# Performance work log

Measured on AMD Instinct MI355X. Metric: run time of the kernel, lower is better.

## Reference

```python
import jax, jax.numpy as jnp
import numpy as np

N = 50000
E = 800000
IN_DIM, HID, HEADS, OUT = 128, 32, 8, 64
NEG_SLOPE = 0.2
EPS = 1e-16


def setup_inputs() -> dict:
    key = jax.random.key(0)
    ks = jax.random.split(key, 10)
    return {
        "x": jax.random.normal(ks[0], (N, IN_DIM), dtype=jnp.float32),
        "edge_index": jax.random.randint(ks[1], (2, E), 0, N, dtype=jnp.int64)
        if jax.config.jax_enable_x64 else jax.random.randint(ks[1], (2, E), 0, N, dtype=jnp.int32),
        "W1": jax.random.normal(ks[2], (HEADS * HID, IN_DIM), dtype=jnp.float32) * 0.1,
        "att_src1": jax.random.normal(ks[3], (HEADS, HID), dtype=jnp.float32) * 0.1,
        "att_dst1": jax.random.normal(ks[4], (HEADS, HID), dtype=jnp.float32) * 0.1,
        "b1": jnp.zeros((HEADS * HID,), dtype=jnp.float32),
        "W2": jax.random.normal(ks[5], (OUT, HEADS * HID), dtype=jnp.float32) * 0.1,
        "att_src2": jax.random.normal(ks[6], (1, OUT), dtype=jnp.float32) * 0.1,
        "att_dst2": jax.random.normal(ks[7], (1, OUT), dtype=jnp.float32) * 0.1,
        "b2": jnp.zeros((OUT,), dtype=jnp.float32),
    }


def _gat_conv(x, src, dst, W, att_src, att_dst, bias, heads, out_dim, concat, n_nodes):
    # x: [N, F_in]; W: [heads*out_dim, F_in]; att_*: [heads, out_dim]
    h = (x @ W.T).reshape(n_nodes, heads, out_dim)      # [N, H, D]
    a_src = jnp.einsum('nhd,hd->nh', h, att_src)         # [N, H]
    a_dst = jnp.einsum('nhd,hd->nh', h, att_dst)
    alpha = jax.nn.leaky_relu(a_src[src] + a_dst[dst], NEG_SLOPE)  # [E, H]
    # segment softmax over edges grouped by destination node
    m = jax.ops.segment_max(alpha, dst, num_segments=n_nodes)
    alpha = jnp.exp(alpha - m[dst])
    s = jax.ops.segment_sum(alpha, dst, num_segments=n_nodes)
    alpha = alpha / (s[dst] + EPS)
    msg = h[src] * alpha[:, :, None]                     # [E, H, D]
    out = jax.ops.segment_sum(msg, dst, num_segments=n_nodes)  # [N, H, D]
    if concat:
        out = out.reshape(n_nodes, heads * out_dim)
    else:
        out = out.mean(axis=1)
    return out + bias


def reference(x, edge_index, W1, att_src1, att_dst1, b1, W2, att_src2, att_dst2, b2):
    n = x.shape[0]
    loop = jnp.arange(n, dtype=edge_index.dtype)
    src = jnp.concatenate([edge_index[0], loop])  # PyG add_self_loops=True
    dst = jnp.concatenate([edge_index[1], loop])
    h = _gat_conv(x, src, dst, W1, att_src1, att_dst1, b1, HEADS, HID, True, n)
    h = jax.nn.relu(h)
    out = _gat_conv(h, src, dst, W2, att_src2, att_dst2, b2, 1, OUT, False, n)
    return out
```

## Files before the change

kernel.cpp:

```cpp
#include <hip/hip_runtime.h>
#include <hip/hip_fp16.h>

#define NN 50000
#define EE 800000
#define ET (EE + NN)
#define IND 128
#define F1 256
#define H1 8
#define D1 32
#define F2 64
#define NEG 0.2f
#define EPSV 1e-16f

#define MG2 391
#define SCB ((ET + 2047) / 2048)
#define BCAP 64

typedef _Float16 half8_t __attribute__((ext_vector_type(8)));
typedef _Float16 half4_t __attribute__((ext_vector_type(4)));
typedef float floatx4 __attribute__((ext_vector_type(4)));

#define W1N4 (256 * 128 / 4)
#define W2N4 (64 * 256 / 4)
#define DEG4 (NN / 4)
#define CVTN (W1N4 + W2N4 + DEG4 + 256)
__global__ void k_cvtW(const float* __restrict__ w1, const float* __restrict__ w2,
                       __half* __restrict__ w1p, __half* __restrict__ w2h,
                       int* __restrict__ deg, const float* __restrict__ as2w,
                       const float* __restrict__ ad2w, float* __restrict__ v2s,
                       float* __restrict__ v2d) {
  int i = blockIdx.x * blockDim.x + threadIdx.x;
  if (i < W1N4) {
    float4 v = *(const float4*)(w1 + (size_t)i * 4);
    int col = i >> 5;
    int kb = (i * 4) & 127;
    int by = col >> 7, t = (col >> 4) & 7, ar = col & 15;
    int kk = kb >> 5, ag = (kb >> 3) & 3, j = kb & 7;
    int fid = (by * 8 + t) * 4 + kk;
    int lane = ag * 16 + ar;
    __half2 p0 = __floats2half2_rn(v.x, v.y);
    __half2 p1 = __floats2half2_rn(v.z, v.w);
    float2 st;
    *(__half2*)&st.x = p0;
    *(__half2*)&st.y = p1;
    *(float2*)(w1p + fid * 512 + lane * 8 + j) = st;
    return;
  }
  i -= W1N4;
  if (i < W2N4) {
    float4 v = *(const float4*)(w2 + (size_t)i * 4);
    __half2 p0 = __floats2half2_rn(v.x, v.y);
    __half2 p1 = __floats2half2_rn(v.z, v.w);
    float2 st;
    *(__half2*)&st.x = p0;
    *(__half2*)&st.y = p1;
    *(float2*)(w2h + (size_t)i * 4) = st;
    return;
  }
  i -= W2N4;
  if (i < DEG4) {
    int4 z = make_int4(0, 0, 0, 0);
    *(int4*)(deg + i * 4) = z;
    return;
  }
  i -= DEG4;
  if (i < 256) {
    float s = 0.f, d = 0.f;
#pragma unroll 8
    for (int c = 0; c < 64; ++c) {
      float w = w2[c * 256 + i];
      s = fmaf(w, as2w[c], s);
      d = fmaf(w, ad2w[c], d);
    }
    v2s[i] = s;
    v2d[i] = d;
  }
}

__global__ __launch_bounds__(256) void k_scg1(const int* __restrict__ ei,
    int* __restrict__ deg, unsigned short* __restrict__ bkt,
    const float* __restrict__ A, const __half* __restrict__ Bp,
    __half* __restrict__ Ch, const float* __restrict__ as1w,
    const float* __restrict__ ad1w, float* __restrict__ as1,
    float* __restrict__ ad1) {
  if (blockIdx.x >= 2 * MG2) {
    int base = (blockIdx.x - 2 * MG2) * 2048 + threadIdx.x * 8;
    if (base >= ET) return;
    if (base + 8 <= EE) {
      int4 s0 = *(const int4*)(ei + base);
      int4 s1 = *(const int4*)(ei + base + 4);
      int4 d0 = *(const int4*)(ei + EE + base);
      int4 d1 = *(const int4*)(ei + EE + base + 4);
      int s[8] = {s0.x, s0.y, s0.z, s0.w, s1.x, s1.y, s1.z, s1.w};
      int d[8] = {d0.x, d0.y, d0.z, d0.w, d1.x, d1.y, d1.z, d1.w};
#pragma unroll
      for (int j = 0; j < 8; ++j) {
        int pos = atomicAdd(&deg[d[j]], 1);
        if (pos < BCAP) bkt[(d[j] << 6) + pos] = (unsigned short)s[j];
      }
    } else {
      for (int j = 0; j < 8; ++j) {
        int e = base + j;
        if (e >= ET) break;
        int ss, dd;
        if (e < EE) { ss = ei[e]; dd = ei[EE + e]; }
        else        { ss = e - EE; dd = ss; }
        int pos = atomicAdd(&deg[dd], 1);
        if (pos < BCAP) bkt[(dd << 6) + pos] = (unsigned short)ss;
      }
    }
    return;
  }
  int bx = blockIdx.x % MG2, by = blockIdx.x / MG2;
  int tid = threadIdx.x;
  int wv = tid >> 6, lane = tid & 63;
  int m0 = bx * 128 + wv * 16;
  int ar = lane & 15, ag = lane >> 4;
  int r0 = m0 + ar;       if (r0 >= NN) r0 = NN - 1;
  int r1 = m0 + 64 + ar;  if (r1 >= NN) r1 = NN - 1;
  const float* A0 = A + (size_t)r0 * IND + ag * 8;
  const float* A1 = A + (size_t)r1 * IND + ag * 8;
  floatx4 acc[2][8];
#pragma unroll
  for (int rt = 0; rt < 2; ++rt)
#pragma unroll
    for (int t = 0; t < 8; ++t) acc[rt][t] = (floatx4){0.f, 0.f, 0.f, 0.f};
#pragma unroll
  for (int kk = 0; kk < 4; ++kk) {
    int k0 = kk * 32;
    float4 a00 = *(const float4*)(A0 + k0);
    float4 a01 = *(const float4*)(A0 + k0 + 4);
    float4 a10 = *(const float4*)(A1 + k0);
    float4 a11 = *(const float4*)(A1 + k0 + 4);
    half8_t af0, af1;
    af0[0] = (_Float16)a00.x; af0[1] = (_Float16)a00.y;
    af0[2] = (_Float16)a00.z; af0[3] = (_Float16)a00.w;
    af0[4] = (_Float16)a01.x; af0[5] = (_Float16)a01.y;
    af0[6] = (_Float16)a01.z; af0[7] = (_Float16)a01.w;
    af1[0] = (_Float16)a10.x; af1[1] = (_Float16)a10.y;
    af1[2] = (_Float16)a10.z; af1[3] = (_Float16)a10.w;
    af1[4] = (_Float16)a11.x; af1[5] = (_Float16)a11.y;
    af1[6] = (_Float16)a11.z; af1[7] = (_Float16)a11.w;
#pragma unroll
    for (int t = 0; t < 8; ++t) {
      int fid = (by * 8 + t) * 4 + kk;
      half8_t bf = *(const half8_t*)(Bp + fid * 512 + lane * 8);
      acc[0][t] = __builtin_amdgcn_mfma_f32_16x16x32_f16(af0, bf, acc[0][t], 0, 0, 0);
      acc[1][t] = __builtin_amdgcn_mfma_f32_16x16x32_f16(af1, bf, acc[1][t], 0, 0, 0);
    }
  }
#pragma unroll
  for (int rt = 0; rt < 2; ++rt)
#pragma unroll
    for (int t = 0; t < 8; ++t) {
      int col = by * 128 + t * 16 + ar;
#pragma unroll
      for (int r = 0; r < 4; ++r) {
        int m = m0 + rt * 64 + ag * 4 + r;
        if (m < NN) Ch[(size_t)m * F1 + col] = __float2half(acc[rt][t][r]);
      }
    }
#pragma unroll
  for (int hp = 0; hp < 4; ++hp) {
    int head = by * 4 + hp;
    float sp[2][4] = {}, dp[2][4] = {};
#pragma unroll
    for (int th = 0; th < 2; ++th) {
      int t = 2 * hp + th;
      float ws = as1w[head * D1 + th * 16 + ar];
      float wd = ad1w[head * D1 + th * 16 + ar];
#pragma unroll
      for (int rt = 0; rt < 2; ++rt)
#pragma unroll
        for (int r = 0; r < 4; ++r) {
          sp[rt][r] = fmaf(acc[rt][t][r], ws, sp[rt][r]);
          dp[rt][r] = fmaf(acc[rt][t][r], wd, dp[rt][r]);
        }
    }
#pragma unroll
    for (int msk = 1; msk < 16; msk <<= 1)
#pragma unroll
      for (int rt = 0; rt < 2; ++rt)
#pragma unroll
        for (int r = 0; r < 4; ++r) {
          sp[rt][r] += __shfl_xor(sp[rt][r], msk);
          dp[rt][r] += __shfl_xor(dp[rt][r], msk);
        }
    if (ar == 0) {
#pragma unroll
      for (int rt = 0; rt < 2; ++rt)
#pragma unroll
        for (int r = 0; r < 4; ++r) {
          int m = m0 + rt * 64 + ag * 4 + r;
          if (m < NN) {
            as1[m * 8 + head] = sp[rt][r];
            ad1[m * 8 + head] = dp[rt][r];
          }
        }
    }
  }
}

__global__ __launch_bounds__(256) void k_agg1(const int* __restrict__ deg,
    const unsigned short* __restrict__ bkt, const __half* __restrict__ feat,
    const float* __restrict__ as_, const float* __restrict__ ad_,
    const float* __restrict__ bias, const float* __restrict__ v2s,
    const float* __restrict__ v2d, __half* __restrict__ outh,
    float* __restrict__ as2, float* __restrict__ ad2) {
  int wid = threadIdx.x >> 6;
  int lane = threadIdx.x & 63;
  int d = blockIdx.x * 4 + wid;
  if (d >= NN) return;
  const int b = lane >> 5;
  const int q = lane & 31;
  const int h = q >> 2;
  const int sw = lane >> 3;
  const int hw = lane & 7;
  const char* fb = (const char*)feat;
  float adw = ad_[d * 8 + hw];
  float acc[8] = {};
  float wsacc = 0.f;
  int p0 = d << 6;
  int dg = deg[d];
  int p1 = p0 + dg;
  int nfull = dg >> 3;
  int p = p0;
  for (int it = 0; it < nfull; ++it, p += 8) {
    int sW = bkt[p + sw];
    float t = as_[sW * 8 + hw] + adw;
    t = (t > 0.f) ? t : NEG * t;
    float w = __expf(t);
    wsacc += w;
    int wbits = __float_as_int(w);
#pragma unroll
    for (int i = 0; i < 4; ++i) {
      int slot = 2 * i + b;
      int se = __builtin_amdgcn_ds_bpermute(slot * 32, sW);
      float wv = __int_as_float(
          __builtin_amdgcn_ds_bpermute((slot * 8 + h) * 4, wbits));
      half8_t f = *(const half8_t*)(fb + ((se << 9) | (q << 4)));
#pragma unroll
      for (int j = 0; j < 8; ++j) acc[j] = fmaf(wv, (float)f[j], acc[j]);
    }
  }
  if (p < p1) {
    int pw = p + sw;
    bool v = pw < p1;
    int sW = bkt[v ? pw : (p1 - 1)];
    float t = as_[sW * 8 + hw] + adw;
    t = (t > 0.f) ? t : NEG * t;
    float w = v ? __expf(t) : 0.f;
    wsacc += w;
    int wbits = __float_as_int(w);
#pragma unroll
    for (int i = 0; i < 4; ++i) {
      int slot = 2 * i + b;
      int se = __builtin_amdgcn_ds_bpermute(slot * 32, sW);
      float wv = __int_as_float(
          __builtin_amdgcn_ds_bpermute((slot * 8 + h) * 4, wbits));
      half8_t f = *(const half8_t*)(fb + ((se << 9) | (q << 4)));
#pragma unroll
      for (int j = 0; j < 8; ++j) acc[j] = fmaf(wv, (float)f[j], acc[j]);
    }
  }
  wsacc += __shfl_xor(wsacc, 8);
  wsacc += __shfl_xor(wsacc, 16);
  wsacc += __shfl_xor(wsacc, 32);
  float wst = __int_as_float(
      __builtin_amdgcn_ds_bpermute(h * 4, __float_as_int(wsacc)));
#pragma unroll
  for (int j = 0; j < 8; ++j) acc[j] += __shfl_xor(acc[j], 32);
  float inv = 1.f / (wst + EPSV);
  float o[8];
#pragma unroll
  for (int j = 0; j < 8; ++j)
    o[j] = fmaxf(fmaf(acc[j], inv, 0.f) + bias[q * 8 + j], 0.f);
  if (b == 0) {
    __half2 packs[4];
#pragma unroll
    for (int j = 0; j < 8; j += 2)
      packs[j >> 1] = __floats2half2_rn(o[j], o[j + 1]);
    *(float4*)(outh + (size_t)d * 256 + q * 8) = *(float4*)packs;
  }
  float s2 = 0.f, d2 = 0.f;
#pragma unroll
  for (int j = 0; j < 8; ++j) {
    s2 = fmaf(o[j], v2s[q * 8 + j], s2);
    d2 = fmaf(o[j], v2d[q * 8 + j], d2);
  }
#pragma unroll
  for (int m = 1; m < 64; m <<= 1) {
    s2 += __shfl_xor(s2, m);
    d2 += __shfl_xor(d2, m);
  }
  if (lane == 0) { as2[d] = 0.5f * s2; ad2[d] = 0.5f * d2; }
}

__global__ __launch_bounds__(256) void k_g2(const __half* __restrict__ A,
    const __half* __restrict__ Bh, __half* __restrict__ Ch) {
  __shared__ __half Bs[64][256 + 8];
  int tid = threadIdx.x;
  const float4* src = (const float4*)Bh;
  for (int i = tid; i < 64 * 256 / 8; i += 256) {
    int row = i / 32, kc = i % 32;
    *(float4*)&Bs[row][kc * 8] = src[i];
  }
  __syncthreads();
  int wv = tid >> 6, lane = tid & 63;
  int m0 = blockIdx.x * 128 + wv * 16;
  int ar = lane & 15, ag = lane >> 4;
  int r0 = m0 + ar;       if (r0 >= NN) r0 = NN - 1;
  int r1 = m0 + 64 + ar;  if (r1 >= NN) r1 = NN - 1;
  const __half* A0 = A + (size_t)r0 * F1 + ag * 8;
  const __half* A1 = A + (size_t)r1 * F1 + ag * 8;
  floatx4 acc[2][4];
#pragma unroll
  for (int rt = 0; rt < 2; ++rt)
#pragma unroll
    for (int t = 0; t < 4; ++t) acc[rt][t] = (floatx4){0.f, 0.f, 0.f, 0.f};
#pragma unroll
  for (int k0 = 0; k0 < F1; k0 += 32) {
    half8_t af0 = *(const half8_t*)(A0 + k0);
    half8_t af1 = *(const half8_t*)(A1 + k0);
#pragma unroll
    for (int t = 0; t < 4; ++t) {
      half8_t bf = *(const half8_t*)&Bs[t * 16 + ar][k0 + ag * 8];
      acc[0][t] = __builtin_amdgcn_mfma_f32_16x16x32_f16(af0, bf, acc[0][t], 0, 0, 0);
      acc[1][t] = __builtin_amdgcn_mfma_f32_16x16x32_f16(af1, bf, acc[1][t], 0, 0, 0);
    }
  }
#pragma unroll
  for (int rt = 0; rt < 2; ++rt)
#pragma unroll
    for (int t = 0; t < 4; ++t) {
      int col = t * 16 + ar;
#pragma unroll
      for (int r = 0; r < 4; ++r) {
        int m = m0 + rt * 64 + ag * 4 + r;
        if (m < NN) Ch[(size_t)m * F2 + col] = __float2half(acc[rt][t][r]);
      }
    }
}

__global__ __launch_bounds__(256) void k_agg2(const int* __restrict__ deg,
    const unsigned short* __restrict__ bkt, const __half* __restrict__ feat,
    const float* __restrict__ as_, const float* __restrict__ ad_,
    const float* __restrict__ bias, float* __restrict__ out) {
  int slice = blockIdx.x & 1;
  int chunk = blockIdx.x >> 1;
  int wid = threadIdx.x >> 6;
  int lane = threadIdx.x & 63;
  int d = chunk * 4 + wid;
  if (d >= NN) return;
  const int b = lane >> 3;
  const int q = lane & 7;
  const char* fb = (const char*)feat + (slice << 6);
  float adv = ad_[d];
  float a0 = 0.f, a1 = 0.f, a2 = 0.f, a3 = 0.f;
  float ws = 0.f;
  int p0 = d << 6;
  int dg = deg[d];
  int p1 = p0 + dg;
  int nfull = dg >> 3;
  int p = p0;
  for (int it = 0; it < nfull; ++it, p += 8) {
    int se = bkt[p + b];
    float t = as_[se] + adv;
    t = (t > 0.f) ? t : NEG * t;
    float w = __expf(t);
    ws += w;
    half4_t f = *(const half4_t*)(fb + ((se << 7) | (q << 3)));
    a0 = fmaf(w, (float)f[0], a0);
    a1 = fmaf(w, (float)f[1], a1);
    a2 = fmaf(w, (float)f[2], a2);
    a3 = fmaf(w, (float)f[3], a3);
  }
  if (p < p1) {
    int pe = p + b;
    bool v = pe < p1;
    int se = bkt[v ? pe : (p1 - 1)];
    float t = as_[se] + adv;
    t = (t > 0.f) ? t : NEG * t;
    float w = v ? __expf(t) : 0.f;
    ws += w;
    half4_t f = *(const half4_t*)(fb + ((se << 7) | (q << 3)));
    a0 = fmaf(w, (float)f[0], a0);
    a1 = fmaf(w, (float)f[1], a1);
    a2 = fmaf(w, (float)f[2], a2);
    a3 = fmaf(w, (float)f[3], a3);
  }
  ws += __shfl_xor(ws, 8); ws += __shfl_xor(ws, 16); ws += __shfl_xor(ws, 32);
  a0 += __shfl_xor(a0, 8); a0 += __shfl_xor(a0, 16); a0 += __shfl_xor(a0, 32);
  a1 += __shfl_xor(a1, 8); a1 += __shfl_xor(a1, 16); a1 += __shfl_xor(a1, 32);
  a2 += __shfl_xor(a2, 8); a2 += __shfl_xor(a2, 16); a2 += __shfl_xor(a2, 32);
  a3 += __shfl_xor(a3, 8); a3 += __shfl_xor(a3, 16); a3 += __shfl_xor(a3, 32);
  if (b == 0) {
    float inv = 1.f / (ws + EPSV);
    int d0 = slice * 32 + q * 4;
    float4 o;
    o.x = fmaf(a0, inv, bias[d0 + 0]);
    o.y = fmaf(a1, inv, bias[d0 + 1]);
    o.z = fmaf(a2, inv, bias[d0 + 2]);
    o.w = fmaf(a3, inv, bias[d0 + 3]);
    *(float4*)(out + (size_t)d * 64 + d0) = o;
  }
}

extern "C" void kernel_launch(void* const* d_in, const int* in_sizes, int n_in,
                              void* d_out, int out_size, void* d_ws, size_t ws_size,
                              hipStream_t stream) {
  const float* x    = (const float*)d_in[0];
  const int*   ei   = (const int*)d_in[1];
  const float* W1   = (const float*)d_in[2];
  const float* as1w = (const float*)d_in[3];
  const float* ad1w = (const float*)d_in[4];
  const float* b1   = (const float*)d_in[5];
  const float* W2   = (const float*)d_in[6];
  const float* as2w = (const float*)d_in[7];
  const float* ad2w = (const float*)d_in[8];
  const float* b2   = (const float*)d_in[9];
  float* out = (float*)d_out;

  char* W = (char*)d_ws;
  __half* h1h = (__half*)W; W += (size_t)NN * 256 * 2;
  __half* h2h = (__half*)W; W += (size_t)NN * 256 * 2;
  __half* hmh = (__half*)W; W += (size_t)NN * 64 * 2;
  __half* W1p = (__half*)W; W += 256 * 128 * 2;
  __half* W2h = (__half*)W; W += 64 * 256 * 2;
  float* as1 = (float*)W; W += (size_t)NN * 8 * 4;
  float* ad1 = (float*)W; W += (size_t)NN * 8 * 4;
  float* as2 = (float*)W; W += (size_t)NN * 4;
  float* ad2 = (float*)W; W += (size_t)NN * 4;
  float* v2s = (float*)W; W += 256 * 4;
  float* v2d = (float*)W; W += 256 * 4;
  int* deg    = (int*)W;  W += (size_t)NN * 4;
  unsigned short* bkt = (unsigned short*)W; W += (size_t)NN * BCAP * 2;

  k_cvtW<<<(CVTN + 255) / 256, 256, 0, stream>>>(W1, W2, W1p, W2h, deg,
                                                 as2w, ad2w, v2s, v2d);
  k_scg1<<<2 * MG2 + SCB, 256, 0, stream>>>(ei, deg, bkt, x, W1p, h1h,
                                            as1w, ad1w, as1, ad1);
  k_agg1<<<(NN + 3) / 4, 256, 0, stream>>>(deg, bkt, h1h, as1, ad1, b1,
                                           v2s, v2d, h2h, as2, ad2);
  k_g2<<<MG2, 256, 0, stream>>>(h2h, W2h, hmh);
  k_agg2<<<2 * ((NN + 3) / 4), 256, 0, stream>>>(deg, bkt, hmh, as2, ad2, b2, out);
}
```

Before: 195.4 us.

## Pre-bin edges by destination range before bucket scatter; widen agg2 to full rows

Adds a k_bin pass that groups edges into 8 destination-range bins using block-local counts and global cursors, packing dst and src into one 32-bit word. The bucket-scatter blocks in k_scg1 then walk each bin, so the degree atomics and bucket writes for neighbouring blocks hit a narrower address range. The aim is better L2 locality for those atomics, paid for by an extra kernel launch and a round trip through the bin buffer. Separately, k_agg2 now has each wave handle all 64 output features with 8-wide half loads instead of splitting every node across two blocks, which halves the index and attention loads per node but doubles the register accumulators.

```diff
diff --git a/kernel.cpp b/kernel.cpp
--- a/kernel.cpp
+++ b/kernel.cpp
@@ -13,22 +13,26 @@
 #define EPSV 1e-16f
 
 #define MG2 391
-#define SCB ((ET + 2047) / 2048)
 #define BCAP 64
+#define NBIN 8
+#define DPB 6250
+#define BINCAP 114688
+#define SB2 56
+#define NSC (NBIN * SB2)
+#define BINB ((ET + 1023) / 1024)
 
 typedef _Float16 half8_t __attribute__((ext_vector_type(8)));
-typedef _Float16 half4_t __attribute__((ext_vector_type(4)));
 typedef float floatx4 __attribute__((ext_vector_type(4)));
 
 #define W1N4 (256 * 128 / 4)
 #define W2N4 (64 * 256 / 4)
 #define DEG4 (NN / 4)
-#define CVTN (W1N4 + W2N4 + DEG4 + 256)
+#define CVTN (W1N4 + W2N4 + DEG4 + 256 + 8)
 __global__ void k_cvtW(const float* __restrict__ w1, const float* __restrict__ w2,
                        __half* __restrict__ w1p, __half* __restrict__ w2h,
                        int* __restrict__ deg, const float* __restrict__ as2w,
                        const float* __restrict__ ad2w, float* __restrict__ v2s,
-                       float* __restrict__ v2d) {
+                       float* __restrict__ v2d, int* __restrict__ gcur) {
   int i = blockIdx.x * blockDim.x + threadIdx.x;
   if (i < W1N4) {
     float4 v = *(const float4*)(w1 + (size_t)i * 4);
@@ -74,44 +78,89 @@
     }
     v2s[i] = s;
     v2d[i] = d;
-  }
-}
-
-__global__ __launch_bounds__(256) void k_scg1(const int* __restrict__ ei,
-    int* __restrict__ deg, unsigned short* __restrict__ bkt,
-    const float* __restrict__ A, const __half* __restrict__ Bp,
-    __half* __restrict__ Ch, const float* __restrict__ as1w,
-    const float* __restrict__ ad1w, float* __restrict__ as1,
-    float* __restrict__ ad1) {
-  if (blockIdx.x >= 2 * MG2) {
-    int base = (blockIdx.x - 2 * MG2) * 2048 + threadIdx.x * 8;
-    if (base >= ET) return;
-    if (base + 8 <= EE) {
-      int4 s0 = *(const int4*)(ei + base);
-      int4 s1 = *(const int4*)(ei + base + 4);
-      int4 d0 = *(const int4*)(ei + EE + base);
-      int4 d1 = *(const int4*)(ei + EE + base + 4);
-      int s[8] = {s0.x, s0.y, s0.z, s0.w, s1.x, s1.y, s1.z, s1.w};
-      int d[8] = {d0.x, d0.y, d0.z, d0.w, d1.x, d1.y, d1.z, d1.w};
+    return;
+  }
+  i -= 256;
+  if (i < 8) gcur[i] = 0;
+}
+
+__global__ __launch_bounds__(256) void k_bin(const int* __restrict__ ei,
+    int* __restrict__ gcur, unsigned int* __restrict__ binbuf) {
+  __shared__ int lcnt[NBIN], lbase[NBIN];
+  if (threadIdx.x < NBIN) lcnt[threadIdx.x] = 0;
+  __syncthreads();
+  int base = blockIdx.x * 1024 + threadIdx.x * 4;
+  int s[4], d[4], bin[4], lpos[4];
+  int nv = 0;
+  if (base + 4 <= EE) {
+    int4 sv = *(const int4*)(ei + base);
+    int4 dv = *(const int4*)(ei + EE + base);
+    s[0] = sv.x; s[1] = sv.y; s[2] = sv.z; s[3] = sv.w;
+    d[0] = dv.x; d[1] = dv.y; d[2] = dv.z; d[3] = dv.w;
+    nv = 4;
+  } else {
+    for (int j = 0; j < 4; ++j) {
+      int e = base + j;
+      if (e < ET) {
+        if (e < EE) { s[nv] = ei[e]; d[nv] = ei[EE + e]; }
+        else        { s[nv] = e - EE; d[nv] = s[nv]; }
+        ++nv;
+      }
+    }
+  }
+  for (int j = 0; j < nv; ++j) {
+    bin[j] = d[j] / DPB;
+    lpos[j] = atomicAdd(&lcnt[bin[j]], 1);
+  }
+  __syncthreads();
+  if (threadIdx.x < NBIN)
+    lbase[threadIdx.x] = atomicAdd(&gcur[threadIdx.x], lcnt[threadIdx.x]);
+  __syncthreads();
+  for (int j = 0; j < nv; ++j) {
+    int idx = lbase[bin[j]] + lpos[j];
+    if (idx < BINCAP)
+      binbuf[(size_t)bin[j] * BINCAP + idx] =
+          ((unsigned)d[j] << 16) | (unsigned)s[j];
+  }
+}
+
+__global__ __launch_bounds__(256) void k_scg1(const unsigned int* __restrict__ binbuf,
+    const int* __restrict__ gcur, int* __restrict__ deg,
+    unsigned short* __restrict__ bkt, const float* __restrict__ A,
+    const __half* __restrict__ Bp, __half* __restrict__ Ch,
+    const float* __restrict__ as1w, const float* __restrict__ ad1w,
+    float* __restrict__ as1, float* __restrict__ ad1) {
+  if (blockIdx.x < NSC) {
+    int cls = blockIdx.x & 7;
+    int chunk = blockIdx.x >> 3;
+    int cnt = gcur[cls];
+    if (cnt > BINCAP) cnt = BINCAP;
+    int base = chunk * 2048 + threadIdx.x * 8;
+    const unsigned int* buf = binbuf + (size_t)cls * BINCAP;
+    if (base + 8 <= cnt) {
+      uint4 a = *(const uint4*)(buf + base);
+      uint4 b = *(const uint4*)(buf + base + 4);
+      unsigned pk[8] = {a.x, a.y, a.z, a.w, b.x, b.y, b.z, b.w};
 #pragma unroll
       for (int j = 0; j < 8; ++j) {
-        int pos = atomicAdd(&deg[d[j]], 1);
-        if (pos < BCAP) bkt[(d[j] << 6) + pos] = (unsigned short)s[j];
+        int dd = pk[j] >> 16, ss = pk[j] & 0xffff;
+        int pos = atomicAdd(&deg[dd], 1);
+        if (pos < BCAP) bkt[(dd << 6) + pos] = (unsigned short)ss;
       }
     } else {
       for (int j = 0; j < 8; ++j) {
         int e = base + j;
-        if (e >= ET) break;
-        int ss, dd;
-        if (e < EE) { ss = ei[e]; dd = ei[EE + e]; }
-        else        { ss = e - EE; dd = ss; }
+        if (e >= cnt) break;
+        unsigned pk = buf[e];
+        int dd = pk >> 16, ss = pk & 0xffff;
         int pos = atomicAdd(&deg[dd], 1);
         if (pos < BCAP) bkt[(dd << 6) + pos] = (unsigned short)ss;
       }
     }
     return;
   }
-  int bx = blockIdx.x % MG2, by = blockIdx.x / MG2;
+  int b2 = blockIdx.x - NSC;
+  int bx = b2 % MG2, by = b2 / MG2;
   int tid = threadIdx.x;
   int wv = tid >> 6, lane = tid & 63;
   int m0 = bx * 128 + wv * 16;
@@ -346,17 +395,15 @@
     const unsigned short* __restrict__ bkt, const __half* __restrict__ feat,
     const float* __restrict__ as_, const float* __restrict__ ad_,
     const float* __restrict__ bias, float* __restrict__ out) {
-  int slice = blockIdx.x & 1;
-  int chunk = blockIdx.x >> 1;
   int wid = threadIdx.x >> 6;
   int lane = threadIdx.x & 63;
-  int d = chunk * 4 + wid;
+  int d = blockIdx.x * 4 + wid;
   if (d >= NN) return;
   const int b = lane >> 3;
   const int q = lane & 7;
-  const char* fb = (const char*)feat + (slice << 6);
+  const char* fb = (const char*)feat;
   float adv = ad_[d];
-  float a0 = 0.f, a1 = 0.f, a2 = 0.f, a3 = 0.f;
+  float acc[8] = {};
   float ws = 0.f;
   int p0 = d << 6;
   int dg = deg[d];
@@ -369,11 +416,9 @@
     t = (t > 0.f) ? t : NEG * t;
     float w = __expf(t);
     ws += w;
-    half4_t f = *(const half4_t*)(fb + ((se << 7) | (q << 3)));
-    a0 = fmaf(w, (float)f[0], a0);
-    a1 = fmaf(w, (float)f[1], a1);
-    a2 = fmaf(w, (float)f[2], a2);
-    a3 = fmaf(w, (float)f[3], a3);
+    half8_t f = *(const half8_t*)(fb + ((se << 7) | (q << 4)));
+#pragma unroll
+    for (int j = 0; j < 8; ++j) acc[j] = fmaf(w, (float)f[j], acc[j]);
   }
   if (p < p1) {
     int pe = p + b;
@@ -383,26 +428,26 @@
     t = (t > 0.f) ? t : NEG * t;
     float w = v ? __expf(t) : 0.f;
     ws += w;
-    half4_t f = *(const half4_t*)(fb + ((se << 7) | (q << 3)));
-    a0 = fmaf(w, (float)f[0], a0);
-    a1 = fmaf(w, (float)f[1], a1);
-    a2 = fmaf(w, (float)f[2], a2);
-    a3 = fmaf(w, (float)f[3], a3);
-  }
-  ws += __shfl_xor(ws, 8); ws += __shfl_xor(ws, 16); ws += __shfl_xor(ws, 32);
-  a0 += __shfl_xor(a0, 8); a0 += __shfl_xor(a0, 16); a0 += __shfl_xor(a0, 32);
-  a1 += __shfl_xor(a1, 8); a1 += __shfl_xor(a1, 16); a1 += __shfl_xor(a1, 32);
-  a2 += __shfl_xor(a2, 8); a2 += __shfl_xor(a2, 16); a2 += __shfl_xor(a2, 32);
-  a3 += __shfl_xor(a3, 8); a3 += __shfl_xor(a3, 16); a3 += __shfl_xor(a3, 32);
+    half8_t f = *(const half8_t*)(fb + ((se << 7) | (q << 4)));
+#pragma unroll
+    for (int j = 0; j < 8; ++j) acc[j] = fmaf(w, (float)f[j], acc[j]);
+  }
+  ws += __shfl_xor(ws, 8);
+  ws += __shfl_xor(ws, 16);
+  ws += __shfl_xor(ws, 32);
+#pragma unroll
+  for (int j = 0; j < 8; ++j) {
+    acc[j] += __shfl_xor(acc[j], 8);
+    acc[j] += __shfl_xor(acc[j], 16);
+    acc[j] += __shfl_xor(acc[j], 32);
+  }
   if (b == 0) {
     float inv = 1.f / (ws + EPSV);
-    int d0 = slice * 32 + q * 4;
-    float4 o;
-    o.x = fmaf(a0, inv, bias[d0 + 0]);
-    o.y = fmaf(a1, inv, bias[d0 + 1]);
-    o.z = fmaf(a2, inv, bias[d0 + 2]);
-    o.w = fmaf(a3, inv, bias[d0 + 3]);
-    *(float4*)(out + (size_t)d * 64 + d0) = o;
+    float o[8];
+#pragma unroll
+    for (int j = 0; j < 8; ++j) o[j] = acc[j] * inv + bias[q * 8 + j];
+    *(float4*)(out + (size_t)d * 64 + q * 8) = *(float4*)&o[0];
+    *(float4*)(out + (size_t)d * 64 + q * 8 + 4) = *(float4*)&o[4];
   }
 }
 
@@ -434,14 +479,17 @@
   float* v2s = (float*)W; W += 256 * 4;
   float* v2d = (float*)W; W += 256 * 4;
   int* deg    = (int*)W;  W += (size_t)NN * 4;
+  int* gcur   = (int*)W;  W += 8 * 4;
+  unsigned int* binbuf = (unsigned int*)W; W += (size_t)NBIN * BINCAP * 4;
   unsigned short* bkt = (unsigned short*)W; W += (size_t)NN * BCAP * 2;
 
   k_cvtW<<<(CVTN + 255) / 256, 256, 0, stream>>>(W1, W2, W1p, W2h, deg,
-                                                 as2w, ad2w, v2s, v2d);
-  k_scg1<<<2 * MG2 + SCB, 256, 0, stream>>>(ei, deg, bkt, x, W1p, h1h,
-                                            as1w, ad1w, as1, ad1);
+                                                 as2w, ad2w, v2s, v2d, gcur);
+  k_bin<<<BINB, 256, 0, stream>>>(ei, gcur, binbuf);
+  k_scg1<<<NSC + 2 * MG2, 256, 0, stream>>>(binbuf, gcur, deg, bkt, x, W1p,
+                                            h1h, as1w, ad1w, as1, ad1);
   k_agg1<<<(NN + 3) / 4, 256, 0, stream>>>(deg, bkt, h1h, as1, ad1, b1,
                                            v2s, v2d, h2h, as2, ad2);
   k_g2<<<MG2, 256, 0, stream>>>(h2h, W2h, hmh);
-  k_agg2<<<2 * ((NN + 3) / 4), 256, 0, stream>>>(deg, bkt, hmh, as2, ad2, b2, out);
-}
+  k_agg2<<<(NN + 3) / 4, 256, 0, stream>>>(deg, bkt, hmh, as2, ad2, b2, out);
+}
```

Measured after the change: 193.4 us. No clear change (-1.0%).

## Split layer-1 features into head-half slices and aggregate per slice

Applied to the files above, without the earlier changes.

Layer-1 GEMM output and attention logits are now stored in two separate half-width slices (4 heads each). The first aggregation kernel launches two blocks per node group, one per slice, gathering 256-byte rows instead of 512-byte rows so each slice's gather working set stays cache-resident. The layer-2 attention logits are accumulated with atomics and zeroed in the conversion kernel. The second aggregation goes the other way, merging its two slice blocks into one block that uses 8-wide loads. Risks are duplicated edge/bucket reads in the first aggregation and atomic contention on the logit buffers.

```diff
diff --git a/kernel.cpp b/kernel.cpp
--- a/kernel.cpp
+++ b/kernel.cpp
@@ -23,12 +23,13 @@
 #define W1N4 (256 * 128 / 4)
 #define W2N4 (64 * 256 / 4)
 #define DEG4 (NN / 4)
-#define CVTN (W1N4 + W2N4 + DEG4 + 256)
+#define AS24 (2 * NN / 4)
+#define CVTN (W1N4 + W2N4 + DEG4 + 256 + AS24)
 __global__ void k_cvtW(const float* __restrict__ w1, const float* __restrict__ w2,
                        __half* __restrict__ w1p, __half* __restrict__ w2h,
                        int* __restrict__ deg, const float* __restrict__ as2w,
                        const float* __restrict__ ad2w, float* __restrict__ v2s,
-                       float* __restrict__ v2d) {
+                       float* __restrict__ v2d, float* __restrict__ as2z) {
   int i = blockIdx.x * blockDim.x + threadIdx.x;
   if (i < W1N4) {
     float4 v = *(const float4*)(w1 + (size_t)i * 4);
@@ -74,6 +75,12 @@
     }
     v2s[i] = s;
     v2d[i] = d;
+    return;
+  }
+  i -= 256;
+  if (i < AS24) {
+    float4 z = make_float4(0.f, 0.f, 0.f, 0.f);
+    *(float4*)(as2z + (size_t)i * 4) = z;
   }
 }
 
@@ -149,15 +156,16 @@
       acc[1][t] = __builtin_amdgcn_mfma_f32_16x16x32_f16(af1, bf, acc[1][t], 0, 0, 0);
     }
   }
+  __half* Chs = Ch + (size_t)by * NN * 128;
 #pragma unroll
   for (int rt = 0; rt < 2; ++rt)
 #pragma unroll
     for (int t = 0; t < 8; ++t) {
-      int col = by * 128 + t * 16 + ar;
+      int col = t * 16 + ar;
 #pragma unroll
       for (int r = 0; r < 4; ++r) {
         int m = m0 + rt * 64 + ag * 4 + r;
-        if (m < NN) Ch[(size_t)m * F1 + col] = __float2half(acc[rt][t][r]);
+        if (m < NN) Chs[(size_t)m * 128 + col] = __float2half(acc[rt][t][r]);
       }
     }
 #pragma unroll
@@ -193,8 +201,8 @@
         for (int r = 0; r < 4; ++r) {
           int m = m0 + rt * 64 + ag * 4 + r;
           if (m < NN) {
-            as1[m * 8 + head] = sp[rt][r];
-            ad1[m * 8 + head] = dp[rt][r];
+            as1[(size_t)by * NN * 4 + m * 4 + hp] = sp[rt][r];
+            ad1[(size_t)by * NN * 4 + m * 4 + hp] = dp[rt][r];
           }
         }
     }
@@ -207,18 +215,21 @@
     const float* __restrict__ bias, const float* __restrict__ v2s,
     const float* __restrict__ v2d, __half* __restrict__ outh,
     float* __restrict__ as2, float* __restrict__ ad2) {
+  int slice = blockIdx.x & 1;
+  int chunk = blockIdx.x >> 1;
   int wid = threadIdx.x >> 6;
   int lane = threadIdx.x & 63;
-  int d = blockIdx.x * 4 + wid;
-  if (d >= NN) return;
+  int d = chunk * 4 + wid;
   const int b = lane >> 5;
   const int q = lane & 31;
-  const int h = q >> 2;
+  const int hq = q >> 3;
   const int sw = lane >> 3;
-  const int hw = lane & 7;
-  const char* fb = (const char*)feat;
-  float adw = ad_[d * 8 + hw];
-  float acc[8] = {};
+  const int hw = lane & 3;
+  const char* fb = (const char*)feat + (size_t)slice * NN * 256;
+  const float* asb = as_ + (size_t)slice * NN * 4;
+  const float* adb = ad_ + (size_t)slice * NN * 4;
+  float adw = adb[d * 4 + hw];
+  float acc[4] = {};
   float wsacc = 0.f;
   int p0 = d << 6;
   int dg = deg[d];
@@ -227,7 +238,7 @@
   int p = p0;
   for (int it = 0; it < nfull; ++it, p += 8) {
     int sW = bkt[p + sw];
-    float t = as_[sW * 8 + hw] + adw;
+    float t = asb[sW * 4 + hw] + adw;
     t = (t > 0.f) ? t : NEG * t;
     float w = __expf(t);
     wsacc += w;
@@ -237,17 +248,19 @@
       int slot = 2 * i + b;
       int se = __builtin_amdgcn_ds_bpermute(slot * 32, sW);
       float wv = __int_as_float(
-          __builtin_amdgcn_ds_bpermute((slot * 8 + h) * 4, wbits));
-      half8_t f = *(const half8_t*)(fb + ((se << 9) | (q << 4)));
-#pragma unroll
-      for (int j = 0; j < 8; ++j) acc[j] = fmaf(wv, (float)f[j], acc[j]);
+          __builtin_amdgcn_ds_bpermute((slot * 8 + hq) * 4, wbits));
+      half4_t f = *(const half4_t*)(fb + ((size_t)se << 8) + (q << 3));
+      acc[0] = fmaf(wv, (float)f[0], acc[0]);
+      acc[1] = fmaf(wv, (float)f[1], acc[1]);
+      acc[2] = fmaf(wv, (float)f[2], acc[2]);
+      acc[3] = fmaf(wv, (float)f[3], acc[3]);
     }
   }
   if (p < p1) {
     int pw = p + sw;
     bool v = pw < p1;
     int sW = bkt[v ? pw : (p1 - 1)];
-    float t = as_[sW * 8 + hw] + adw;
+    float t = asb[sW * 4 + hw] + adw;
     t = (t > 0.f) ? t : NEG * t;
     float w = v ? __expf(t) : 0.f;
     wsacc += w;
@@ -257,43 +270,48 @@
       int slot = 2 * i + b;
       int se = __builtin_amdgcn_ds_bpermute(slot * 32, sW);
       float wv = __int_as_float(
-          __builtin_amdgcn_ds_bpermute((slot * 8 + h) * 4, wbits));
-      half8_t f = *(const half8_t*)(fb + ((se << 9) | (q << 4)));
-#pragma unroll
-      for (int j = 0; j < 8; ++j) acc[j] = fmaf(wv, (float)f[j], acc[j]);
+          __builtin_amdgcn_ds_bpermute((slot * 8 + hq) * 4, wbits));
+      half4_t f = *(const half4_t*)(fb + ((size_t)se << 8) + (q << 3));
+      acc[0] = fmaf(wv, (float)f[0], acc[0]);
+      acc[1] = fmaf(wv, (float)f[1], acc[1]);
+      acc[2] = fmaf(wv, (float)f[2], acc[2]);
+      acc[3] = fmaf(wv, (float)f[3], acc[3]);
     }
   }
   wsacc += __shfl_xor(wsacc, 8);
   wsacc += __shfl_xor(wsacc, 16);
   wsacc += __shfl_xor(wsacc, 32);
   float wst = __int_as_float(
-      __builtin_amdgcn_ds_bpermute(h * 4, __float_as_int(wsacc)));
-#pragma unroll
-  for (int j = 0; j < 8; ++j) acc[j] += __shfl_xor(acc[j], 32);
+      __builtin_amdgcn_ds_bpermute(hq * 4, __float_as_int(wsacc)));
+#pragma unroll
+  for (int j = 0; j < 4; ++j) acc[j] += __shfl_xor(acc[j], 32);
   float inv = 1.f / (wst + EPSV);
-  float o[8];
-#pragma unroll
-  for (int j = 0; j < 8; ++j)
-    o[j] = fmaxf(fmaf(acc[j], inv, 0.f) + bias[q * 8 + j], 0.f);
+  int dim0 = slice * 128 + q * 4;
+  float o[4];
+#pragma unroll
+  for (int j = 0; j < 4; ++j)
+    o[j] = fmaxf(fmaf(acc[j], inv, 0.f) + bias[dim0 + j], 0.f);
   if (b == 0) {
-    __half2 packs[4];
-#pragma unroll
-    for (int j = 0; j < 8; j += 2)
-      packs[j >> 1] = __floats2half2_rn(o[j], o[j + 1]);
-    *(float4*)(outh + (size_t)d * 256 + q * 8) = *(float4*)packs;
+    __half2 pk[2];
+    pk[0] = __floats2half2_rn(o[0], o[1]);
+    pk[1] = __floats2half2_rn(o[2], o[3]);
+    *(float2*)(outh + (size_t)d * 256 + dim0) = *(float2*)pk;
   }
   float s2 = 0.f, d2 = 0.f;
 #pragma unroll
-  for (int j = 0; j < 8; ++j) {
-    s2 = fmaf(o[j], v2s[q * 8 + j], s2);
-    d2 = fmaf(o[j], v2d[q * 8 + j], d2);
+  for (int j = 0; j < 4; ++j) {
+    s2 = fmaf(o[j], v2s[dim0 + j], s2);
+    d2 = fmaf(o[j], v2d[dim0 + j], d2);
   }
 #pragma unroll
   for (int m = 1; m < 64; m <<= 1) {
     s2 += __shfl_xor(s2, m);
     d2 += __shfl_xor(d2, m);
   }
-  if (lane == 0) { as2[d] = 0.5f * s2; ad2[d] = 0.5f * d2; }
+  if (lane == 0) {
+    atomicAdd(&as2[d], 0.5f * s2);
+    atomicAdd(&ad2[d], 0.5f * d2);
+  }
 }
 
 __global__ __launch_bounds__(256) void k_g2(const __half* __restrict__ A,
@@ -346,17 +364,15 @@
     const unsigned short* __restrict__ bkt, const __half* __restrict__ feat,
     const float* __restrict__ as_, const float* __restrict__ ad_,
     const float* __restrict__ bias, float* __restrict__ out) {
-  int slice = blockIdx.x & 1;
-  int chunk = blockIdx.x >> 1;
   int wid = threadIdx.x >> 6;
   int lane = threadIdx.x & 63;
-  int d = chunk * 4 + wid;
+  int d = blockIdx.x * 4 + wid;
   if (d >= NN) return;
   const int b = lane >> 3;
   const int q = lane & 7;
-  const char* fb = (const char*)feat + (slice << 6);
+  const char* fb = (const char*)feat;
   float adv = ad_[d];
-  float a0 = 0.f, a1 = 0.f, a2 = 0.f, a3 = 0.f;
+  float acc[8] = {};
   float ws = 0.f;
   int p0 = d << 6;
   int dg = deg[d];
@@ -369,11 +385,9 @@
     t = (t > 0.f) ? t : NEG * t;
     float w = __expf(t);
     ws += w;
-    half4_t f = *(const half4_t*)(fb + ((se << 7) | (q << 3)));
-    a0 = fmaf(w, (float)f[0], a0);
-    a1 = fmaf(w, (float)f[1], a1);
-    a2 = fmaf(w, (float)f[2], a2);
-    a3 = fmaf(w, (float)f[3], a3);
+    half8_t f = *(const half8_t*)(fb + ((se << 7) | (q << 4)));
+#pragma unroll
+    for (int j = 0; j < 8; ++j) acc[j] = fmaf(w, (float)f[j], acc[j]);
   }
   if (p < p1) {
     int pe = p + b;
@@ -383,26 +397,26 @@
     t = (t > 0.f) ? t : NEG * t;
     float w = v ? __expf(t) : 0.f;
     ws += w;
-    half4_t f = *(const half4_t*)(fb + ((se << 7) | (q << 3)));
-    a0 = fmaf(w, (float)f[0], a0);
-    a1 = fmaf(w, (float)f[1], a1);
-    a2 = fmaf(w, (float)f[2], a2);
-    a3 = fmaf(w, (float)f[3], a3);
-  }
-  ws += __shfl_xor(ws, 8); ws += __shfl_xor(ws, 16); ws += __shfl_xor(ws, 32);
-  a0 += __shfl_xor(a0, 8); a0 += __shfl_xor(a0, 16); a0 += __shfl_xor(a0, 32);
-  a1 += __shfl_xor(a1, 8); a1 += __shfl_xor(a1, 16); a1 += __shfl_xor(a1, 32);
-  a2 += __shfl_xor(a2, 8); a2 += __shfl_xor(a2, 16); a2 += __shfl_xor(a2, 32);
-  a3 += __shfl_xor(a3, 8); a3 += __shfl_xor(a3, 16); a3 += __shfl_xor(a3, 32);
+    half8_t f = *(const half8_t*)(fb + ((se << 7) | (q << 4)));
+#pragma unroll
+    for (int j = 0; j < 8; ++j) acc[j] = fmaf(w, (float)f[j], acc[j]);
+  }
+  ws += __shfl_xor(ws, 8);
+  ws += __shfl_xor(ws, 16);
+  ws += __shfl_xor(ws, 32);
+#pragma unroll
+  for (int j = 0; j < 8; ++j) {
+    acc[j] += __shfl_xor(acc[j], 8);
+    acc[j] += __shfl_xor(acc[j], 16);
+    acc[j] += __shfl_xor(acc[j], 32);
+  }
   if (b == 0) {
     float inv = 1.f / (ws + EPSV);
-    int d0 = slice * 32 + q * 4;
-    float4 o;
-    o.x = fmaf(a0, inv, bias[d0 + 0]);
-    o.y = fmaf(a1, inv, bias[d0 + 1]);
-    o.z = fmaf(a2, inv, bias[d0 + 2]);
-    o.w = fmaf(a3, inv, bias[d0 + 3]);
-    *(float4*)(out + (size_t)d * 64 + d0) = o;
+    float o[8];
+#pragma unroll
+    for (int j = 0; j < 8; ++j) o[j] = acc[j] * inv + bias[q * 8 + j];
+    *(float4*)(out + (size_t)d * 64 + q * 8) = *(float4*)&o[0];
+    *(float4*)(out + (size_t)d * 64 + q * 8 + 4) = *(float4*)&o[4];
   }
 }
 
@@ -422,13 +436,13 @@
   float* out = (float*)d_out;
 
   char* W = (char*)d_ws;
-  __half* h1h = (__half*)W; W += (size_t)NN * 256 * 2;
+  __half* h1s = (__half*)W; W += (size_t)2 * NN * 128 * 2;
   __half* h2h = (__half*)W; W += (size_t)NN * 256 * 2;
   __half* hmh = (__half*)W; W += (size_t)NN * 64 * 2;
   __half* W1p = (__half*)W; W += 256 * 128 * 2;
   __half* W2h = (__half*)W; W += 64 * 256 * 2;
-  float* as1 = (float*)W; W += (size_t)NN * 8 * 4;
-  float* ad1 = (float*)W; W += (size_t)NN * 8 * 4;
+  float* as1 = (float*)W; W += (size_t)2 * NN * 4 * 4;
+  float* ad1 = (float*)W; W += (size_t)2 * NN * 4 * 4;
   float* as2 = (float*)W; W += (size_t)NN * 4;
   float* ad2 = (float*)W; W += (size_t)NN * 4;
   float* v2s = (float*)W; W += 256 * 4;
@@ -437,11 +451,11 @@
   unsigned short* bkt = (unsigned short*)W; W += (size_t)NN * BCAP * 2;
 
   k_cvtW<<<(CVTN + 255) / 256, 256, 0, stream>>>(W1, W2, W1p, W2h, deg,
-                                                 as2w, ad2w, v2s, v2d);
-  k_scg1<<<2 * MG2 + SCB, 256, 0, stream>>>(ei, deg, bkt, x, W1p, h1h,
+                                                 as2w, ad2w, v2s, v2d, as2);
+  k_scg1<<<2 * MG2 + SCB, 256, 0, stream>>>(ei, deg, bkt, x, W1p, h1s,
                                             as1w, ad1w, as1, ad1);
-  k_agg1<<<(NN + 3) / 4, 256, 0, stream>>>(deg, bkt, h1h, as1, ad1, b1,
-                                           v2s, v2d, h2h, as2, ad2);
+  k_agg1<<<2 * 12500, 256, 0, stream>>>(deg, bkt, h1s, as1, ad1, b1,
+                                        v2s, v2d, h2h, as2, ad2);
   k_g2<<<MG2, 256, 0, stream>>>(h2h, W2h, hmh);
-  k_agg2<<<2 * ((NN + 3) / 4), 256, 0, stream>>>(deg, bkt, hmh, as2, ad2, b2, out);
-}
+  k_agg2<<<(NN + 3) / 4, 256, 0, stream>>>(deg, bkt, hmh, as2, ad2, b2, out);
+}
```

New measurement: 181.1 us. 1.08x faster.
